# Kernel optimization log

Hardware: AMD Instinct MI355X
Metric: run time of the kernel (lower is better)

The kernel has to match this reference:

```python
import jax, jax.numpy as jnp
import numpy as np

N = 8192      # batch*seq_len (batch=4, seq_len=2048)
DK = 256
DV = 256


def setup_inputs() -> dict:
    key = jax.random.key(0)
    ks = jax.random.split(key, 9)
    s = 1.0 / np.sqrt(DK)
    return {
        "q": jax.random.normal(ks[0], (N, DK), jnp.float32),
        "k": jax.random.normal(ks[1], (N, DK), jnp.float32),
        "v": jax.random.normal(ks[2], (N, DV), jnp.float32),
        "Wq": jax.random.normal(ks[3], (DK, DK), jnp.float32) * s,
        "bq": jnp.zeros((DK,), jnp.float32),
        "Wk": jax.random.normal(ks[4], (DK, DK), jnp.float32) * s,
        "bk": jnp.zeros((DK,), jnp.float32),
        "Wv": jax.random.normal(ks[5], (DV, DV), jnp.float32) * s,
        "bv": jnp.zeros((DV,), jnp.float32),
        "seq_len": 2048,
    }


def reference(q, k, v, Wq, bq, Wk, bk, Wv, bv, seq_len):
    # torch Linear: y = x @ W.T + b
    Q = q @ Wq.T + bq                       # [N, dk]
    K = k @ Wk.T + bk                       # [N, dk]
    V = v @ Wv.T + bv                       # [N, dv]
    sqrt_dk = jnp.sqrt(jnp.asarray(DK, Q.dtype))
    score = (Q @ K.T) / sqrt_dk             # [N, N] — attends over ALL tokens
    # original reshapes to (B, S, N) and softmaxes over dim=-1, which is
    # identical to row-wise softmax on the [N, N] score matrix
    attn = jax.nn.softmax(score, axis=-1)   # [N, N]
    return attn @ V                          # [N, dv]
```

## Files before the change

kernel.cpp:

```cpp
#include <hip/hip_runtime.h>
#include <hip/hip_bf16.h>


typedef __attribute__((ext_vector_type(8))) short short8;
typedef __attribute__((ext_vector_type(4))) short short4v;
typedef __attribute__((ext_vector_type(4))) float f32x4;
typedef __attribute__((ext_vector_type(4))) float float4v;
typedef __attribute__((ext_vector_type(16))) float f32x16;

#define MFMA16 __builtin_amdgcn_mfma_f32_16x16x32_bf16
#define MFMA32 __builtin_amdgcn_mfma_f32_32x32x16_bf16

namespace {
constexpr int kN = 8192;
constexpr int kD = 256;
constexpr int kKVB = 32;
}

__device__ __forceinline__ unsigned cvtpk_bf16(float lo, float hi) {
  unsigned d;
  asm("v_cvt_pk_bf16_f32 %0, %1, %2" : "=v"(d) : "v"(lo), "v"(hi));
  return d;
}

__device__ __forceinline__ short4v pk4(float a, float b, float c, float d) {
  union { unsigned u[2]; short4v s; } p;
  p.u[0] = cvtpk_bf16(a, b);
  p.u[1] = cvtpk_bf16(c, d);
  return p.s;
}

__device__ __forceinline__ void plswap(unsigned& a, unsigned& b) {
  auto r = __builtin_amdgcn_permlane32_swap(a, b, false, false);
  a = r[0]; b = r[1];
}
__device__ __forceinline__ float xhalf_sum(float x) {
  unsigned u = __builtin_bit_cast(unsigned, x), v = u;
  plswap(u, v);
  return __builtin_bit_cast(float, u) + __builtin_bit_cast(float, v);
}

__device__ __forceinline__ void gll16(const short* g, const short* lp) {
  __builtin_amdgcn_global_load_lds(
      (const __attribute__((address_space(1))) void*)g,
      (__attribute__((address_space(3))) void*)lp, 16, 0, 0);
}

__device__ __forceinline__ void softmax_pack(f32x16& sacc, short8& pa0, short8& pa1,
                                             float& lsum) {
  float psum = 0.f;
#pragma unroll
  for (int r = 0; r < 16; ++r) {
    sacc[r] = __builtin_amdgcn_exp2f(sacc[r]);
    psum += sacc[r];
  }
  {
    unsigned A0 = cvtpk_bf16(sacc[0], sacc[1]);
    unsigned A1 = cvtpk_bf16(sacc[2], sacc[3]);
    unsigned B0 = cvtpk_bf16(sacc[4], sacc[5]);
    unsigned B1 = cvtpk_bf16(sacc[6], sacc[7]);
    plswap(A0, B0);
    plswap(A1, B1);
    union { unsigned u[4]; short8 s8; } pu;
    pu.u[0] = A0; pu.u[1] = A1; pu.u[2] = B0; pu.u[3] = B1;
    pa0 = pu.s8;
  }
  {
    unsigned A0 = cvtpk_bf16(sacc[8], sacc[9]);
    unsigned A1 = cvtpk_bf16(sacc[10], sacc[11]);
    unsigned B0 = cvtpk_bf16(sacc[12], sacc[13]);
    unsigned B1 = cvtpk_bf16(sacc[14], sacc[15]);
    plswap(A0, B0);
    plswap(A1, B1);
    union { unsigned u[4]; short8 s8; } pu;
    pu.u[0] = A0; pu.u[1] = A1; pu.u[2] = B0; pu.u[3] = B1;
    pa1 = pu.s8;
  }
  lsum += xhalf_sum(psum);
}

__global__ __launch_bounds__(256, 2) void proj_kernel(
    const float* __restrict__ qx, const float* __restrict__ kx, const float* __restrict__ vx,
    const float* __restrict__ Wq, const float* __restrict__ bq,
    const float* __restrict__ Wk, const float* __restrict__ bk,
    const float* __restrict__ Wv, const float* __restrict__ bv,
    short* __restrict__ Qimg, short* __restrict__ Kimg, short* __restrict__ Vimg)
{
  const int mode = blockIdx.y;
  const float* X; const float* W; const float* B;
  if (mode == 0)      { X = qx; W = Wq; B = bq; }
  else if (mode == 1) { X = kx; W = Wk; B = bk; }
  else                { X = vx; W = Wv; B = bv; }

  const int nb = blockIdx.x * 64;

  __shared__ short XA[64][264];
  __shared__ short WB[64][264];

  const int t  = threadIdx.x;
  const int c4 = t & 63;
  const int r0 = t >> 6;

#pragma unroll
  for (int p = 0; p < 16; ++p) {
    const int r = p * 4 + r0;
    float4v xv = *(const float4v*)(X + (size_t)(nb + r) * kD + c4 * 4);
    *(short4v*)(&XA[r][c4 * 4]) = pk4(xv[0], xv[1], xv[2], xv[3]);
  }

  float4v wreg[16];
#pragma unroll
  for (int p = 0; p < 16; ++p)
    wreg[p] = *(const float4v*)(W + (size_t)(p * 4 + r0) * kD + c4 * 4);

  const int w  = t >> 6;
  const int l  = t & 63;
  const int lr = l & 15;
  const int g  = l >> 4;

  for (int obi = 0; obi < 4; ++obi) {
    __syncthreads();
#pragma unroll
    for (int p = 0; p < 16; ++p)
      *(short4v*)(&WB[p * 4 + r0][c4 * 4]) = pk4(wreg[p][0], wreg[p][1], wreg[p][2], wreg[p][3]);
    __syncthreads();
    if (obi < 3) {
#pragma unroll
      for (int p = 0; p < 16; ++p)
        wreg[p] = *(const float4v*)(W + (size_t)((obi + 1) * 64 + p * 4 + r0) * kD + c4 * 4);
    }

    const f32x4 vzero = {0.f, 0.f, 0.f, 0.f};
    f32x4 acc[4];
#pragma unroll
    for (int ct = 0; ct < 4; ++ct) acc[ct] = vzero;

    if (mode == 2) {
#pragma unroll
      for (int s = 0; s < 8; ++s) {
        short8 af = *(const short8*)(&XA[w * 16 + lr][s * 32 + g * 8]);
#pragma unroll
        for (int ct = 0; ct < 4; ++ct) {
          short8 bf = *(const short8*)(&WB[ct * 16 + lr][s * 32 + g * 8]);
          acc[ct] = MFMA16(af, bf, acc[ct], 0, 0, 0);
        }
      }
#pragma unroll
      for (int ct = 0; ct < 4; ++ct) {
        const int o = obi * 64 + ct * 16 + lr;
        const float bias = B[o];
        const int n0 = nb + w * 16 + g * 4;
        const size_t idx = (size_t)(n0 >> 5) * 8192 + (size_t)(o >> 5) * 1024
                         + (size_t)((n0 >> 4) & 1) * 512 + (size_t)((n0 >> 3) & 1) * 256
                         + (size_t)(o & 31) * 8 + (n0 & 7);
        *(short4v*)(Vimg + idx) = pk4(acc[ct][0] + bias, acc[ct][1] + bias,
                                      acc[ct][2] + bias, acc[ct][3] + bias);
      }
    } else {
#pragma unroll
      for (int s = 0; s < 8; ++s) {
        short8 af = *(const short8*)(&WB[w * 16 + lr][s * 32 + g * 8]);
#pragma unroll
        for (int ct = 0; ct < 4; ++ct) {
          short8 bf = *(const short8*)(&XA[ct * 16 + lr][s * 32 + g * 8]);
          acc[ct] = MFMA16(af, bf, acc[ct], 0, 0, 0);
        }
      }
      short* Out = (mode == 0) ? Qimg : Kimg;
      const float sc = (mode == 0) ? (0.0625f * 1.44269504089f) : 1.0f;
      const int o0 = obi * 64 + w * 16 + g * 4;
      const float4v bv4 = *(const float4v*)(B + o0);
#pragma unroll
      for (int ct = 0; ct < 4; ++ct) {
        const int n = nb + ct * 16 + lr;
        const size_t idx = (size_t)(n >> 5) * 8192 + (size_t)(o0 >> 4) * 512
                         + (size_t)((o0 >> 3) & 1) * 256 + (size_t)(n & 31) * 8 + (o0 & 7);
        *(short4v*)(Out + idx) = pk4((acc[ct][0] + bv4[0]) * sc, (acc[ct][1] + bv4[1]) * sc,
                                     (acc[ct][2] + bv4[2]) * sc, (acc[ct][3] + bv4[3]) * sc);
      }
    }
  }
}

template<int SPLIT>
__global__ __launch_bounds__(512, 2) void flash_kernel(
    const short* __restrict__ Qimg, const short* __restrict__ Kimg, const short* __restrict__ Vimg,
    short* __restrict__ Ops, float* __restrict__ Ls)
{
  constexpr int kTiles = (kN / SPLIT) / kKVB;
  constexpr int kPairs = kTiles / 2;
  const int linear = (int)blockIdx.x;
  int sp, qb;
  if (SPLIT == 8) { sp = linear & 7; qb = linear >> 3; }
  else { const int xcd = linear & 7; sp = xcd >> 1; qb = ((linear >> 3) << 1) | (xcd & 1); }
  const int kvblk0 = sp * kTiles;

  __shared__ short sbuf[4 * 8192 + 5 * 8192];

  const int t = threadIdx.x;
  const int w = t >> 6, l = t & 63;
  const int hf = l >> 5;
  const int lc = l & 31;

  auto stageK = [&](int tile, int slot) {
    const short* kg = Kimg + (size_t)(kvblk0 + tile) * 8192 + w * 512 + l * 8;
    const short* d = sbuf + slot * 8192 + w * 512;
    gll16(kg, d);
    gll16(kg + 4096, d + 4096);
  };
  auto stageV = [&](int tile, int slot) {
    const short* vg = Vimg + (size_t)(kvblk0 + tile) * 8192 + w * 512 + l * 8;
    const short* d = sbuf + 32768 + slot * 8192 + w * 512;
    gll16(vg, d);
    gll16(vg + 4096, d + 4096);
  };

  stageK(0, 0); stageV(0, 0);
  stageK(1, 1); stageV(1, 1);

  short8 qf[16];
  {
    const short* qsrc = Qimg + (size_t)(qb * 8 + w) * 8192 + l * 8;
#pragma unroll
    for (int ks = 0; ks < 16; ++ks) qf[ks] = *(const short8*)(qsrc + ks * 512);
  }

  f32x16 oacc[8];
#pragma unroll
  for (int dvt = 0; dvt < 8; ++dvt)
#pragma unroll
    for (int r = 0; r < 16; ++r) oacc[dvt][r] = 0.f;
  float lsum = 0.f;
  short8 pa0, pa1;

  asm volatile("s_waitcnt vmcnt(0)" ::: "memory");
  __syncthreads();

  auto qk_pv = [&](int kslot, int vslot, f32x16& sacc) {
    const short* kb = sbuf + kslot * 8192 + l * 8;
    const short* vb = sbuf + 32768 + vslot * 8192 + l * 8;
    __builtin_amdgcn_s_setprio(1);
#pragma unroll
    for (int ks = 0; ks < 16; ++ks) {
      short8 kf = *(const short8*)(kb + ks * 512);
      sacc = MFMA32(kf, qf[ks], sacc, 0, 0, 0);
      short8 vf = *(const short8*)(vb + ks * 512);
      oacc[ks >> 1] = MFMA32((ks & 1) ? pa1 : pa0, vf, oacc[ks >> 1], 0, 0, 0);
    }
    __builtin_amdgcn_s_setprio(0);
  };

  {
    if (kPairs > 1) { stageK(2, 2); stageV(2, 2); stageK(3, 3); stageV(3, 3); }
    f32x16 sacc;
#pragma unroll
    for (int r = 0; r < 16; ++r) sacc[r] = 0.f;
    const short* kb = sbuf + l * 8;
    __builtin_amdgcn_s_setprio(1);
#pragma unroll
    for (int ks = 0; ks < 16; ++ks) {
      short8 kf = *(const short8*)(kb + ks * 512);
      sacc = MFMA32(kf, qf[ks], sacc, 0, 0, 0);
    }
    __builtin_amdgcn_s_setprio(0);
    softmax_pack(sacc, pa0, pa1, lsum);

    f32x16 sacc1;
#pragma unroll
    for (int r = 0; r < 16; ++r) sacc1[r] = 0.f;
    qk_pv(1, 0, sacc1);
    softmax_pack(sacc1, pa0, pa1, lsum);

    asm volatile("s_waitcnt vmcnt(0)" ::: "memory");
    __syncthreads();
  }

  int v_m1 = 1;
  for (int tt = 1; tt < kPairs; ++tt) {
    const int a = 2 * tt;
    const int v0 = (v_m1 == 4) ? 0 : v_m1 + 1;
    const int v1 = (v0 == 4) ? 0 : v0 + 1;
    if (tt + 1 < kPairs) {
      const int v2 = (v1 == 4) ? 0 : v1 + 1;
      const int v3 = (v2 == 4) ? 0 : v2 + 1;
      stageK(a + 2, (a + 2) & 3); stageV(a + 2, v2);
      stageK(a + 3, (a + 3) & 3); stageV(a + 3, v3);
    }

    f32x16 sacc;
#pragma unroll
    for (int r = 0; r < 16; ++r) sacc[r] = 0.f;
    qk_pv(a & 3, v_m1, sacc);
    softmax_pack(sacc, pa0, pa1, lsum);

    f32x16 sacc1;
#pragma unroll
    for (int r = 0; r < 16; ++r) sacc1[r] = 0.f;
    qk_pv((a + 1) & 3, v0, sacc1);
    softmax_pack(sacc1, pa0, pa1, lsum);

    if (tt + 1 < kPairs) {
      asm volatile("s_waitcnt vmcnt(0)" ::: "memory");
      __syncthreads();
    }
    v_m1 = v1;
  }

  {
    const short* vb = sbuf + 32768 + v_m1 * 8192 + l * 8;
    __builtin_amdgcn_s_setprio(1);
#pragma unroll
    for (int ks = 0; ks < 16; ++ks) {
      short8 vf = *(const short8*)(vb + ks * 512);
      oacc[ks >> 1] = MFMA32((ks & 1) ? pa1 : pa0, vf, oacc[ks >> 1], 0, 0, 0);
    }
    __builtin_amdgcn_s_setprio(0);
  }

  const float rl = 1.0f / lsum;
  float cs[16];
#pragma unroll
  for (int r = 0; r < 16; ++r)
    cs[r] = __shfl(rl, (r & 3) + 8 * (r >> 2) + 4 * hf) * 4096.f;
  const int qrow0 = qb * 256 + w * 32;
#pragma unroll
  for (int dvt = 0; dvt < 8; ++dvt)
#pragma unroll
    for (int r = 0; r < 16; ++r) {
      const int q = qrow0 + (r & 3) + 8 * (r >> 2) + 4 * hf;
      float x = oacc[dvt][r] * cs[r];
      x = fminf(fmaxf(x, -32767.f), 32767.f);
      Ops[((size_t)sp * kN + q) * kD + dvt * 32 + lc] = (short)(int)rintf(x);
    }
  if (l < 32) Ls[(size_t)sp * kN + qrow0 + l] = lsum;
}

template<int SPLIT>
__global__ __launch_bounds__(256) void merge_kernel(
    const short* __restrict__ Ops, const float* __restrict__ Ls, float* __restrict__ out)
{
  const int t = threadIdx.x;
  const int qrow = blockIdx.x * 8 + (t >> 5);
  const int d0 = (t & 31) * 8;
  float li[SPLIT];
  float denom = 0.f;
#pragma unroll
  for (int s = 0; s < SPLIT; ++s) { li[s] = Ls[(size_t)s * kN + qrow]; denom += li[s]; }
  float n[8];
#pragma unroll
  for (int j = 0; j < 8; ++j) n[j] = 0.f;
#pragma unroll
  for (int s = 0; s < SPLIT; ++s) {
    const short8 u = *(const short8*)(Ops + ((size_t)s * kN + qrow) * kD + d0);
#pragma unroll
    for (int j = 0; j < 8; ++j) n[j] += li[s] * (float)u[j];
  }
  const float inv = 1.0f / (denom * 4096.f);
  float4v o0, o1;
#pragma unroll
  for (int j = 0; j < 4; ++j) { o0[j] = n[j] * inv; o1[j] = n[4 + j] * inv; }
  *(float4v*)(out + (size_t)qrow * kD + d0)     = o0;
  *(float4v*)(out + (size_t)qrow * kD + d0 + 4) = o1;
}

extern "C" void kernel_launch(void* const* d_in, const int* in_sizes, int n_in,
                              void* d_out, int out_size, void* d_ws, size_t ws_size,
                              hipStream_t stream)
{
  const float* q  = (const float*)d_in[0];
  const float* k  = (const float*)d_in[1];
  const float* v  = (const float*)d_in[2];
  const float* Wq = (const float*)d_in[3];
  const float* bq = (const float*)d_in[4];
  const float* Wk = (const float*)d_in[5];
  const float* bk = (const float*)d_in[6];
  const float* Wv = (const float*)d_in[7];
  const float* bv = (const float*)d_in[8];

  char* ws = (char*)d_ws;
  short* Qimg = (short*)(ws);
  short* Kimg = (short*)(ws + ((size_t)4 << 20));
  short* Vimg = (short*)(ws + ((size_t)8 << 20));
  const size_t opOff = (size_t)12 << 20;
  short* Ops = (short*)(ws + opOff);

  proj_kernel<<<dim3(kN / 64, 3), 256, 0, stream>>>(
      q, k, v, Wq, bq, Wk, bk, Wv, bv, Qimg, Kimg, Vimg);

  const size_t opBytes8 = (size_t)8 * kN * kD * 2;
  const size_t need8 = opOff + opBytes8 + (size_t)8 * kN * 4;
  if (ws_size >= need8) {
    float* Ls = (float*)(ws + opOff + opBytes8);
    flash_kernel<8><<<dim3(256), 512, 0, stream>>>(Qimg, Kimg, Vimg, Ops, Ls);
    merge_kernel<8><<<dim3(kN / 8), 256, 0, stream>>>(Ops, Ls, (float*)d_out);
  } else {
    const size_t opBytes4 = (size_t)4 * kN * kD * 2;
    float* Ls = (float*)(ws + opOff + opBytes4);
    flash_kernel<4><<<dim3(128), 512, 0, stream>>>(Qimg, Kimg, Vimg, Ops, Ls);
    merge_kernel<4><<<dim3(kN / 8), 256, 0, stream>>>(Ops, Ls, (float*)d_out);
  }
}
```

Measured before the change: 95.50 us.

## Stagger KV tile order between two wave groups to desynchronize LDS access

Splits the eight waves into two groups that walk each pair of KV tiles in opposite order. The second group computes QK for the odd tile first and defers its PV, with an extra register pair to hold those probabilities. A sixth V buffer slot is added so deferred PV reads stay valid under the new modulo-6 slot mapping. The aim is to stop all waves hitting the same LDS tiles and MFMA phases at the same moment, so memory and MFMA work overlap better. In exchange it costs more LDS, adds per-wave branching and register pressure, and introduces a fixed per-pair sync structure.

```diff
diff --git a/kernel.cpp b/kernel.cpp
--- a/kernel.cpp
+++ b/kernel.cpp
@@ -195,28 +195,29 @@
   else { const int xcd = linear & 7; sp = xcd >> 1; qb = ((linear >> 3) << 1) | (xcd & 1); }
   const int kvblk0 = sp * kTiles;
 
-  __shared__ short sbuf[4 * 8192 + 5 * 8192];
+  __shared__ short sbuf[4 * 8192 + 6 * 8192];
 
   const int t = threadIdx.x;
   const int w = t >> 6, l = t & 63;
   const int hf = l >> 5;
   const int lc = l & 31;
-
-  auto stageK = [&](int tile, int slot) {
+  const bool grpA = (w < 4);
+
+  auto stageK = [&](int tile) {
     const short* kg = Kimg + (size_t)(kvblk0 + tile) * 8192 + w * 512 + l * 8;
-    const short* d = sbuf + slot * 8192 + w * 512;
+    const short* d = sbuf + (tile & 3) * 8192 + w * 512;
     gll16(kg, d);
     gll16(kg + 4096, d + 4096);
   };
-  auto stageV = [&](int tile, int slot) {
+  auto stageV = [&](int tile) {
     const short* vg = Vimg + (size_t)(kvblk0 + tile) * 8192 + w * 512 + l * 8;
-    const short* d = sbuf + 32768 + slot * 8192 + w * 512;
+    const short* d = sbuf + 32768 + (tile % 6) * 8192 + w * 512;
     gll16(vg, d);
     gll16(vg + 4096, d + 4096);
   };
 
-  stageK(0, 0); stageV(0, 0);
-  stageK(1, 1); stageV(1, 1);
+  stageK(0); stageV(0);
+  stageK(1); stageV(1);
 
   short8 qf[16];
   {
@@ -232,10 +233,21 @@
     for (int r = 0; r < 16; ++r) oacc[dvt][r] = 0.f;
   float lsum = 0.f;
   short8 pa0, pa1;
+  short8 pb0, pb1;
 
   asm volatile("s_waitcnt vmcnt(0)" ::: "memory");
   __syncthreads();
 
+  auto qk_only = [&](int kslot, f32x16& sacc) {
+    const short* kb = sbuf + kslot * 8192 + l * 8;
+    __builtin_amdgcn_s_setprio(1);
+#pragma unroll
+    for (int ks = 0; ks < 16; ++ks) {
+      short8 kf = *(const short8*)(kb + ks * 512);
+      sacc = MFMA32(kf, qf[ks], sacc, 0, 0, 0);
+    }
+    __builtin_amdgcn_s_setprio(0);
+  };
   auto qk_pv = [&](int kslot, int vslot, f32x16& sacc) {
     const short* kb = sbuf + kslot * 8192 + l * 8;
     const short* vb = sbuf + 32768 + vslot * 8192 + l * 8;
@@ -249,73 +261,54 @@
     }
     __builtin_amdgcn_s_setprio(0);
   };
-
-  {
-    if (kPairs > 1) { stageK(2, 2); stageV(2, 2); stageK(3, 3); stageV(3, 3); }
-    f32x16 sacc;
-#pragma unroll
-    for (int r = 0; r < 16; ++r) sacc[r] = 0.f;
-    const short* kb = sbuf + l * 8;
+  auto pv_only = [&](int vslot, const short8& p0, const short8& p1) {
+    const short* vb = sbuf + 32768 + vslot * 8192 + l * 8;
     __builtin_amdgcn_s_setprio(1);
 #pragma unroll
     for (int ks = 0; ks < 16; ++ks) {
-      short8 kf = *(const short8*)(kb + ks * 512);
-      sacc = MFMA32(kf, qf[ks], sacc, 0, 0, 0);
+      short8 vf = *(const short8*)(vb + ks * 512);
+      oacc[ks >> 1] = MFMA32((ks & 1) ? p1 : p0, vf, oacc[ks >> 1], 0, 0, 0);
     }
     __builtin_amdgcn_s_setprio(0);
-    softmax_pack(sacc, pa0, pa1, lsum);
-
-    f32x16 sacc1;
-#pragma unroll
-    for (int r = 0; r < 16; ++r) sacc1[r] = 0.f;
-    qk_pv(1, 0, sacc1);
-    softmax_pack(sacc1, pa0, pa1, lsum);
+  };
+
+  for (int tt = 0; tt < kPairs; ++tt) {
+    const int a = 2 * tt, b = a + 1;
+    if (a + 2 < kTiles) { stageK(a + 2); stageV(a + 2); }
+    if (a + 3 < kTiles) { stageK(a + 3); stageV(a + 3); }
+
+    if (grpA) {
+      f32x16 s1;
+#pragma unroll
+      for (int r = 0; r < 16; ++r) s1[r] = 0.f;
+      if (tt == 0) qk_only(a & 3, s1);
+      else         qk_pv(a & 3, (a - 1) % 6, s1);
+      softmax_pack(s1, pa0, pa1, lsum);
+      f32x16 s2;
+#pragma unroll
+      for (int r = 0; r < 16; ++r) s2[r] = 0.f;
+      qk_pv(b & 3, a % 6, s2);
+      softmax_pack(s2, pa0, pa1, lsum);
+    } else {
+      f32x16 s1;
+#pragma unroll
+      for (int r = 0; r < 16; ++r) s1[r] = 0.f;
+      qk_only(b & 3, s1);
+      softmax_pack(s1, pb0, pb1, lsum);
+      f32x16 s2;
+#pragma unroll
+      for (int r = 0; r < 16; ++r) s2[r] = 0.f;
+      if (tt == 0) qk_only(a & 3, s2);
+      else         qk_pv(a & 3, (a - 2) % 6, s2);
+      softmax_pack(s2, pa0, pa1, lsum);
+      pv_only(b % 6, pb0, pb1);
+    }
 
     asm volatile("s_waitcnt vmcnt(0)" ::: "memory");
     __syncthreads();
   }
 
-  int v_m1 = 1;
-  for (int tt = 1; tt < kPairs; ++tt) {
-    const int a = 2 * tt;
-    const int v0 = (v_m1 == 4) ? 0 : v_m1 + 1;
-    const int v1 = (v0 == 4) ? 0 : v0 + 1;
-    if (tt + 1 < kPairs) {
-      const int v2 = (v1 == 4) ? 0 : v1 + 1;
-      const int v3 = (v2 == 4) ? 0 : v2 + 1;
-      stageK(a + 2, (a + 2) & 3); stageV(a + 2, v2);
-      stageK(a + 3, (a + 3) & 3); stageV(a + 3, v3);
-    }
-
-    f32x16 sacc;
-#pragma unroll
-    for (int r = 0; r < 16; ++r) sacc[r] = 0.f;
-    qk_pv(a & 3, v_m1, sacc);
-    softmax_pack(sacc, pa0, pa1, lsum);
-
-    f32x16 sacc1;
-#pragma unroll
-    for (int r = 0; r < 16; ++r) sacc1[r] = 0.f;
-    qk_pv((a + 1) & 3, v0, sacc1);
-    softmax_pack(sacc1, pa0, pa1, lsum);
-
-    if (tt + 1 < kPairs) {
-      asm volatile("s_waitcnt vmcnt(0)" ::: "memory");
-      __syncthreads();
-    }
-    v_m1 = v1;
-  }
-
-  {
-    const short* vb = sbuf + 32768 + v_m1 * 8192 + l * 8;
-    __builtin_amdgcn_s_setprio(1);
-#pragma unroll
-    for (int ks = 0; ks < 16; ++ks) {
-      short8 vf = *(const short8*)(vb + ks * 512);
-      oacc[ks >> 1] = MFMA32((ks & 1) ? pa1 : pa0, vf, oacc[ks >> 1], 0, 0, 0);
-    }
-    __builtin_amdgcn_s_setprio(0);
-  }
+  pv_only(grpA ? (kTiles - 1) % 6 : (kTiles - 2) % 6, pa0, pa1);
 
   const float rl = 1.0f / lsum;
   float cs[16];
```

New measurement: 97.72 us. +2.3%, slower.
